# Kernel tuning notes

Measured on AMD Instinct MI355X. Metric: run time of the kernel, lower is better.

## Reference

```python
import jax, jax.numpy as jnp
import numpy as np

B, N, M = 8, 1024, 64          # graphs, ops/graph, machines/graph
OPF, MF = 16, 8                # raw feature dims
H, D, L = 8, 64, 3             # heads, head dim, HGT layers
F = H * D                      # 512 = hidden_dim * num_heads
KC = 8                         # compatible machines per op
NOP, NM = B * N, B * M
EPS = 1e-5


def _graph_ln(x, w, b):
    # PyG LayerNorm(mode='graph') with batch=None: scalar mean/std over the whole tensor
    x = x - x.mean()
    return x / (x.std() + EPS) * w + b


def _seg_softmax(a, idx, n):
    amax = jax.ops.segment_max(a, idx, num_segments=n)
    amax = jnp.where(jnp.isfinite(amax), amax, 0.0)
    ex = jnp.exp(a - amax[idx])
    s = jax.ops.segment_sum(ex, idx, num_segments=n)
    return ex / (s[idx] + 1e-16)


def _forward(op_x, machine_x, W_emb_op, b_emb_op, W_emb_m, b_emb_m,
             opn_w, opn_b, mn_w, mn_b, Wk, bk, Wq, bq, Wv, bv,
             A_rel, M_rel, p_rel, W_out, b_out, skip, ln_w, ln_b,
             ei_precedes, ei_canproc, ei_compat):
    x_op = _graph_ln(op_x @ W_emb_op + b_emb_op, opn_w, opn_b)
    x_m = _graph_ln(machine_x @ W_emb_m + b_emb_m, mn_w, mn_b)
    s0, d0 = ei_precedes   # op -> op
    s1, d1 = ei_canproc    # machine -> op
    s2, d2 = ei_compat     # op -> machine
    scale = 1.0 / jnp.sqrt(jnp.float32(D))
    for l in range(L):
        k_op = (x_op @ Wk[l, 0] + bk[l, 0]).reshape(NOP, H, D)
        q_op = (x_op @ Wq[l, 0] + bq[l, 0]).reshape(NOP, H, D)
        v_op = (x_op @ Wv[l, 0] + bv[l, 0]).reshape(NOP, H, D)
        k_m = (x_m @ Wk[l, 1] + bk[l, 1]).reshape(NM, H, D)
        q_m = (x_m @ Wq[l, 1] + bq[l, 1]).reshape(NM, H, D)
        v_m = (x_m @ Wv[l, 1] + bv[l, 1]).reshape(NM, H, D)
        # relation-specific per-head transforms (a_rel/m_rel of HGTConv)
        k0 = jnp.einsum('nhd,hde->nhe', k_op, A_rel[l, 0]); v0 = jnp.einsum('nhd,hde->nhe', v_op, M_rel[l, 0])
        k1 = jnp.einsum('nhd,hde->nhe', k_m, A_rel[l, 1]);  v1 = jnp.einsum('nhd,hde->nhe', v_m, M_rel[l, 1])
        k2 = jnp.einsum('nhd,hde->nhe', k_op, A_rel[l, 2]); v2 = jnp.einsum('nhd,hde->nhe', v_op, M_rel[l, 2])
        # attention into op nodes: joint softmax over both incoming edge types
        a0 = (q_op[d0] * k0[s0]).sum(-1) * p_rel[l, 0] * scale   # [E0,H]
        a1 = (q_op[d1] * k1[s1]).sum(-1) * p_rel[l, 1] * scale   # [E1,H]
        a_op = jnp.concatenate([a0, a1]); dd = jnp.concatenate([d0, d1])
        w = _seg_softmax(a_op, dd, NOP)
        msg = jnp.concatenate([v0[s0], v1[s1]]) * w[:, :, None]
        agg_op = jax.ops.segment_sum(msg, dd, num_segments=NOP).reshape(NOP, F)
        # attention into machine nodes
        a2 = (q_m[d2] * k2[s2]).sum(-1) * p_rel[l, 2] * scale
        w2 = _seg_softmax(a2, d2, NM)
        agg_m = jax.ops.segment_sum(v2[s2] * w2[:, :, None], d2, num_segments=NM).reshape(NM, F)
        # output projection + learned skip gate (HGTConv internals)
        o_op = jax.nn.gelu(agg_op, approximate=False) @ W_out[l, 0] + b_out[l, 0]
        o_m = jax.nn.gelu(agg_m, approximate=False) @ W_out[l, 1] + b_out[l, 1]
        g_op = jax.nn.sigmoid(skip[l, 0]); g_m = jax.nn.sigmoid(skip[l, 1])
        o_op = g_op * o_op + (1.0 - g_op) * x_op
        o_m = g_m * o_m + (1.0 - g_m) * x_m
        # wrapper residual + dropout(eval=identity) + graph layer norm
        x_op = _graph_ln(o_op + x_op, ln_w[l], ln_b[l])
        x_m = _graph_ln(o_m + x_m, ln_w[l], ln_b[l])
    fea_j = x_op.reshape(B, N, F)
    fea_m = x_m.reshape(B, M, F)
    return fea_j, fea_m, fea_j.mean(1, keepdims=True), fea_m.mean(1, keepdims=True)


def setup_inputs() -> dict:
    key = jax.random.key(0)
    ks = jax.random.split(key, 12)
    rng = np.random.default_rng(0)
    ids = np.arange(NOP).reshape(B, N)
    src0 = ids[:, :-1].ravel(); dst0 = ids[:, 1:].ravel()
    mach = rng.integers(0, M, size=(B, N, KC)) + (np.arange(B) * M)[:, None, None]
    ops = np.broadcast_to(ids[:, :, None], (B, N, KC))
    ei_precedes = jnp.asarray(np.stack([src0, dst0]), dtype=jnp.int32)
    ei_canproc = jnp.asarray(np.stack([mach.ravel(), ops.ravel()]), dtype=jnp.int32)
    ei_compat = jnp.asarray(np.stack([ops.ravel(), mach.ravel()]), dtype=jnp.int32)
    n = lambda k, sh, s=0.05: jax.random.normal(k, sh, dtype=jnp.float32) * s
    return dict(
        op_x=n(ks[0], (NOP, OPF), 1.0),
        machine_x=n(ks[1], (NM, MF), 1.0),
        W_emb_op=n(ks[2], (OPF, F)), b_emb_op=jnp.zeros((F,), jnp.float32),
        W_emb_m=n(ks[3], (MF, F)), b_emb_m=jnp.zeros((F,), jnp.float32),
        opn_w=jnp.ones((F,), jnp.float32), opn_b=jnp.zeros((F,), jnp.float32),
        mn_w=jnp.ones((F,), jnp.float32), mn_b=jnp.zeros((F,), jnp.float32),
        Wk=n(ks[4], (L, 2, F, F)), bk=jnp.zeros((L, 2, F), jnp.float32),
        Wq=n(ks[5], (L, 2, F, F)), bq=jnp.zeros((L, 2, F), jnp.float32),
        Wv=n(ks[6], (L, 2, F, F)), bv=jnp.zeros((L, 2, F), jnp.float32),
        A_rel=n(ks[7], (L, 3, H, D, D)), M_rel=n(ks[8], (L, 3, H, D, D)),
        p_rel=jnp.ones((L, 3, H), jnp.float32),
        W_out=n(ks[9], (L, 2, F, F)), b_out=jnp.zeros((L, 2, F), jnp.float32),
        skip=jnp.ones((L, 2), jnp.float32),
        ln_w=jnp.ones((L, F), jnp.float32), ln_b=jnp.zeros((L, F), jnp.float32),
        ei_precedes=ei_precedes, ei_canproc=ei_canproc, ei_compat=ei_compat,
    )


def reference(op_x, machine_x, W_emb_op, b_emb_op, W_emb_m, b_emb_m,
              opn_w, opn_b, mn_w, mn_b, Wk, bk, Wq, bq, Wv, bv,
              A_rel, M_rel, p_rel, W_out, b_out, skip, ln_w, ln_b,
              ei_precedes, ei_canproc, ei_compat):
    return _forward(op_x, machine_x, W_emb_op, b_emb_op, W_emb_m, b_emb_m,
                    opn_w, opn_b, mn_w, mn_b, Wk, bk, Wq, bq, Wv, bv,
                    A_rel, M_rel, p_rel, W_out, b_out, skip, ln_w, ln_b,
                    ei_precedes, ei_canproc, ei_compat)
```

## Files before the change

### kernel.cpp

```cpp
#include <hip/hip_runtime.h>

typedef unsigned short u16;
typedef __attribute__((ext_vector_type(4))) float floatx4;
typedef __attribute__((ext_vector_type(8))) short shortx8;
typedef __attribute__((ext_vector_type(4))) short shortx4;

#define NOPS 8192
#define NMS  512
#define CQ   2560
#define CM   1536
#define NE2  65536
#define TOPC (NOPS*512)
#define TMC  (NMS*512)

__device__ __forceinline__ float bf2f(u16 u){ return __uint_as_float(((unsigned)u)<<16); }
__device__ __forceinline__ u16 f2bf(float f){
  unsigned u = __float_as_uint(f);
  u += 0x7FFFu + ((u>>16)&1u);
  return (u16)(u>>16);
}
__device__ __forceinline__ float wred(float v){
  #pragma unroll
  for (int o=32;o;o>>=1) v += __shfl_xor(v,o,64);
  return v;
}
__device__ __forceinline__ float wredmax(float v){
  #pragma unroll
  for (int o=32;o;o>>=1) v = fmaxf(v, __shfl_xor(v,o,64));
  return v;
}
__device__ __forceinline__ float geluf(float x){
  return 0.5f*x*(1.f+erff(x*0.70710678118654752f));
}
__device__ __forceinline__ void block_stat_out2(float s, float s2, float* pstat, int slot){
  __shared__ float sb[8];
  s = wred(s); s2 = wred(s2);
  int wv = threadIdx.x >> 6;
  if ((threadIdx.x & 63) == 0){ sb[wv*2] = s; sb[wv*2+1] = s2; }
  __syncthreads();
  if (threadIdx.x == 0){
    float a = 0.f, b = 0.f;
    int nw = blockDim.x >> 6;
    for (int i=0;i<nw;++i){ a += sb[i*2]; b += sb[i*2+1]; }
    pstat[slot*2]   = a;
    pstat[slot*2+1] = b;
  }
}

__global__ __launch_bounds__(256) void cnt2_k(const int* __restrict__ s1, float* __restrict__ Ct,
                                              float* __restrict__ Cn){
  int idx = blockIdx.x*256 + threadIdx.x;
  int n = idx >> 6, l = idx & 63;
  const int* row = s1 + n*8;
  int cnt = 0;
  #pragma unroll
  for (int j=0;j<8;++j) cnt += ((row[j] & 63) == l);
  float f = (float)cnt;
  Cn[(size_t)n*64 + l] = f;
  int b = n >> 10, nl = n & 1023;
  Ct[(size_t)((b<<6) + l)*1024 + nl] = f;
}

__global__ __launch_bounds__(256) void tw_k(const float* __restrict__ Wout, const float* __restrict__ Wq,
                                            u16* __restrict__ Wout_t, u16* __restrict__ Wc_op_t,
                                            u16* __restrict__ Wc_m_t){
  __shared__ u16 t[64][65];
  int g = blockIdx.x;
  const float* s; u16* d;
  if (g < 6){
    s = Wout + (size_t)g*262144;
    d = Wout_t + (size_t)g*262144;
  } else {
    int blk = g - 6; int l = blk >> 1, side = blk & 1;
    s = Wq + (size_t)blk*262144;
    d = side ? (Wc_m_t + (size_t)l*CM*512) : (Wc_op_t + (size_t)l*CQ*512);
  }
  int kb = blockIdx.y*64, nb = blockIdx.z*64;
  int tx = threadIdx.x & 63, ty4 = threadIdx.x >> 6;
  #pragma unroll 4
  for (int p=0;p<16;++p){
    int k = ty4 + p*4;
    t[k][tx] = f2bf(s[(size_t)(kb+k)*512 + nb + tx]);
  }
  __syncthreads();
  #pragma unroll 4
  for (int p=0;p<16;++p){
    int n = ty4 + p*4;
    d[(size_t)(nb+n)*512 + kb + tx] = t[tx][n];
  }
}

__global__ void qb_k(const float* __restrict__ bq, float* bias_op, float* bias_m){
  int i = blockIdx.x*blockDim.x + threadIdx.x;
  if (i >= 3072) return;
  int l = i >> 10, side = (i >> 9) & 1, f = i & 511;
  float v = bq[(l*2+side)*512 + f];
  if (side==0) bias_op[l*CQ + f] = v; else bias_m[l*CM + f] = v;
}

__global__ __launch_bounds__(256) void combine3_k(const float* __restrict__ Wk, const float* __restrict__ Wv,
                                                  const float* __restrict__ Ar, const float* __restrict__ Mr,
                                                  u16* __restrict__ Wc_op_t, u16* __restrict__ Wc_m_t){
  __shared__ u16 As[64*72];
  __shared__ u16 Bs[128*72];
  int gx = blockIdx.x;
  int l = gx/48; int rem = gx - l*48; int s = rem >> 3; int h = rem & 7;
  int side = (s < 4) ? 0 : 1;
  int r = (s < 4) ? (s+1) : (s-3);
  int useK = side==0 ? (s==0 || s==2) : (s==4);
  int rel  = side==0 ? ((s<2)?0:2) : 1;
  const float* W   = (useK ? Wk : Wv) + (size_t)(l*2+side)*262144;
  const float* Rel = (useK ? Ar : Mr) + ((size_t)(l*3+rel)*8 + h)*4096;
  int h64 = h*64;
  u16* Wt = side ? (Wc_m_t + (size_t)l*CM*512) : (Wc_op_t + (size_t)l*CQ*512);
  int rbase = r*512 + h64;
  int cc0 = blockIdx.y * 128;
  int tid = threadIdx.x, lane = tid & 63, wave = tid >> 6;
  {
    int d = tid >> 2, e0 = (tid & 3) * 16;
    #pragma unroll
    for (int j=0;j<16;++j) As[(e0+j)*72 + d] = f2bf(Rel[d*64 + e0 + j]);
  }
  {
    int ccl = tid >> 1, d0 = (tid & 1) * 32;
    const float* src = W + (size_t)(cc0+ccl)*512 + h64 + d0;
    #pragma unroll
    for (int j=0;j<32;j+=4){
      floatx4 v = *(const floatx4*)(src + j);
      shortx4 sv;
      #pragma unroll
      for (int e=0;e<4;++e) sv[e] = (short)f2bf(v[e]);
      *(shortx4*)(Bs + ccl*72 + d0 + j) = sv;
    }
  }
  __syncthreads();
  int wm = wave & 1, wn = wave >> 1;
  int mrow = lane & 15, quad = lane >> 4;
  floatx4 acc[2][4];
  #pragma unroll
  for (int a=0;a<2;++a)
    #pragma unroll
    for (int b=0;b<4;++b) acc[a][b] = (floatx4){0.f,0.f,0.f,0.f};
  #pragma unroll
  for (int ks=0; ks<2; ++ks){
    shortx8 af[2], bf[4];
    #pragma unroll
    for (int mt=0;mt<2;++mt) af[mt] = *(const shortx8*)(As + (wm*32 + mt*16 + mrow)*72 + ks*32 + quad*8);
    #pragma unroll
    for (int nt=0;nt<4;++nt) bf[nt] = *(const shortx8*)(Bs + (wn*64 + nt*16 + mrow)*72 + ks*32 + quad*8);
    #pragma unroll
    for (int mt=0;mt<2;++mt)
      #pragma unroll
      for (int nt=0;nt<4;++nt)
        acc[mt][nt] = __builtin_amdgcn_mfma_f32_16x16x32_bf16(af[mt], bf[nt], acc[mt][nt], 0, 0, 0);
  }
  #pragma unroll
  for (int mt=0;mt<2;++mt){
    #pragma unroll
    for (int nt=0;nt<4;++nt){
      int ccl = wn*64 + nt*16 + mrow;
      #pragma unroll
      for (int r2=0;r2<4;++r2){
        int e = wm*32 + mt*16 + quad*4 + r2;
        Wt[(size_t)(rbase + e)*512 + cc0 + ccl] = f2bf(acc[mt][nt][r2]);
      }
    }
  }
}
__global__ void cbias_k(const float* __restrict__ bk, const float* __restrict__ bv,
                        const float* __restrict__ Ar, const float* __restrict__ Mr,
                        float* bias_op, float* bias_m){
  int gx = blockIdx.x; int e = threadIdx.x;
  int l = gx/48; int rem = gx - l*48; int s = rem >> 3; int h = rem & 7;
  int side = (s < 4) ? 0 : 1;
  int r = (s < 4) ? (s+1) : (s-3);
  int useK = side==0 ? (s==0 || s==2) : (s==4);
  int rel  = side==0 ? ((s<2)?0:2) : 1;
  const float* bb  = (useK ? bk : bv) + (size_t)(l*2+side)*512 + h*64;
  const float* Rel = (useK ? Ar : Mr) + ((size_t)(l*3+rel)*8 + h)*4096;
  float acc = 0.f;
  for (int d=0; d<64; ++d) acc += bb[d]*Rel[d*64 + e];
  float* bias = side ? (bias_m + l*CM) : (bias_op + l*CQ);
  bias[r*512 + h*64 + e] = acc;
}

__global__ __launch_bounds__(256) void embed2_k(const float* __restrict__ Xop, const float* __restrict__ Wop,
                                                const float* __restrict__ bop, float* __restrict__ Yop,
                                                const float* __restrict__ Xm, const float* __restrict__ Wm,
                                                const float* __restrict__ bm_, float* __restrict__ Ym,
                                                float* pstat, float* pstat_m){
  int bid = blockIdx.x;
  const float *X, *W, *bias; float *Y, *ps; int K, total, nb, lb;
  if (bid < 1024){ X=Xop; W=Wop; bias=bop; Y=Yop; ps=pstat;   K=16; total=TOPC; nb=1024; lb=bid; }
  else           { X=Xm;  W=Wm;  bias=bm_; Y=Ym;  ps=pstat_m; K=8;  total=TMC;  nb=128;  lb=bid-1024; }
  float s = 0.f, s2 = 0.f;
  for (int idx = lb*256 + threadIdx.x; idx < total; idx += nb*256){
    int n = idx >> 9, f = idx & 511;
    float v = bias[f];
    for (int c=0;c<K;++c) v += X[n*K+c] * W[c*512+f];
    Y[idx] = v;
    s += v; s2 += v*v;
  }
  block_stat_out2(s, s2, ps, lb);
}

__global__ __launch_bounds__(256) void ln2_k(const float* __restrict__ src_op, float* __restrict__ dst_op,
                                             u16* __restrict__ dbf_op, const float* __restrict__ w_op,
                                             const float* __restrict__ b_op,
                                             const float* __restrict__ src_m, float* __restrict__ dst_m,
                                             u16* __restrict__ dbf_m, const float* __restrict__ w_m,
                                             const float* __restrict__ b_m,
                                             const float* __restrict__ pstat, const float* __restrict__ pstat_m,
                                             int nbo, int nbm){
  int bid = blockIdx.x;
  const float *src, *w, *b, *ps; float* dst; u16* dbf; int total4, nb, lb, nblk; float inv_n;
  if (bid < 1024){ src=src_op; dst=dst_op; dbf=dbf_op; w=w_op; b=b_op; ps=pstat;
                   total4=TOPC/4; nb=1024; lb=bid; nblk=nbo; inv_n=1.f/TOPC; }
  else           { src=src_m;  dst=dst_m;  dbf=dbf_m;  w=w_m;  b=b_m;  ps=pstat_m;
                   total4=TMC/4;  nb=128;  lb=bid-1024; nblk=nbm; inv_n=1.f/TMC; }
  __shared__ float sb[8];
  __shared__ float mr[2];
  float s = 0.f, s2 = 0.f;
  for (int i = threadIdx.x; i < nblk; i += 256){ s += ps[2*i]; s2 += ps[2*i+1]; }
  s = wred(s); s2 = wred(s2);
  int wv = threadIdx.x >> 6;
  if ((threadIdx.x & 63) == 0){ sb[wv*2] = s; sb[wv*2+1] = s2; }
  __syncthreads();
  if (threadIdx.x == 0){
    float a = 0.f, bsum = 0.f;
    for (int i=0;i<4;++i){ a += sb[i*2]; bsum += sb[i*2+1]; }
    float mean = a * inv_n;
    float var  = fmaxf(bsum * inv_n - mean*mean, 0.f);
    mr[0] = mean;
    mr[1] = 1.f/(sqrtf(var) + 1e-5f);
  }
  __syncthreads();
  float mean = mr[0], rinv = mr[1];
  const floatx4* s4 = (const floatx4*)src;
  floatx4* d4 = (floatx4*)dst;
  shortx4* db4 = (shortx4*)dbf;
  const floatx4* w4 = (const floatx4*)w;
  const floatx4* b4 = (const floatx4*)b;
  for (int i = lb*256 + threadIdx.x; i < total4; i += nb*256){
    int f = i & 127;
    floatx4 v = s4[i], wv2 = w4[f], bv = b4[f];
    shortx4 sv;
    #pragma unroll
    for (int e=0;e<4;++e){ v[e] = (v[e]-mean)*rinv*wv2[e] + bv[e]; sv[e] = (short)f2bf(v[e]); }
    d4[i] = v;
    db4[i] = sv;
  }
}

__device__ __forceinline__ void gemm_gate_core(u16* As, u16* Bs, const u16* __restrict__ A,
                                               const u16* __restrict__ Bt,
                                               const float* __restrict__ xr, const float* __restrict__ bo,
                                               const float* __restrict__ sk, float* __restrict__ Y,
                                               float* pstat, int slot, int bx, int by){
  const int tid = threadIdx.x;
  const int lane = tid & 63, wave = tid >> 6;
  const int bm = by * 128, bn = bx * 128;
  const int wm = wave & 1, wn = wave >> 1;
  const int mrow = lane & 15, quad = lane >> 4;
  const u16* Ab = A + (size_t)bm*512;
  const u16* Bb = Bt + (size_t)bn*512;
  floatx4 acc[4][4];
  #pragma unroll
  for (int a=0;a<4;++a)
    #pragma unroll
    for (int b=0;b<4;++b) acc[a][b] = (floatx4){0.f,0.f,0.f,0.f};
  const int r0 = tid >> 2, c0 = (tid & 3) * 8;
  const int r1 = (tid+256) >> 2, c1 = ((tid+256) & 3) * 8;
  const int lds0 = wave*512;
  const int lds1 = wave*512 + 2048;
  for (int k0 = 0; k0 < 512; k0 += 32){
    __builtin_amdgcn_global_load_lds((const __attribute__((address_space(1))) void*)(Ab + (size_t)r0*512 + k0 + c0),
                                     (__attribute__((address_space(3))) void*)(As + lds0), 16, 0, 0);
    __builtin_amdgcn_global_load_lds((const __attribute__((address_space(1))) void*)(Ab + (size_t)r1*512 + k0 + c1),
                                     (__attribute__((address_space(3))) void*)(As + lds1), 16, 0, 0);
    __builtin_amdgcn_global_load_lds((const __attribute__((address_space(1))) void*)(Bb + (size_t)r0*512 + k0 + c0),
                                     (__attribute__((address_space(3))) void*)(Bs + lds0), 16, 0, 0);
    __builtin_amdgcn_global_load_lds((const __attribute__((address_space(1))) void*)(Bb + (size_t)r1*512 + k0 + c1),
                                     (__attribute__((address_space(3))) void*)(Bs + lds1), 16, 0, 0);
    __syncthreads();
    shortx8 af[4], bf[4];
    #pragma unroll
    for (int mt=0;mt<4;++mt) af[mt] = *(const shortx8*)(As + (wm*64 + mt*16 + mrow)*32 + quad*8);
    #pragma unroll
    for (int nt=0;nt<4;++nt) bf[nt] = *(const shortx8*)(Bs + (wn*64 + nt*16 + mrow)*32 + quad*8);
    #pragma unroll
    for (int mt=0;mt<4;++mt)
      #pragma unroll
      for (int nt=0;nt<4;++nt)
        acc[mt][nt] = __builtin_amdgcn_mfma_f32_16x16x32_bf16(af[mt], bf[nt], acc[mt][nt], 0, 0, 0);
    __syncthreads();
  }
  float g = 1.f/(1.f+expf(-(*sk)));
  float s = 0.f, s2 = 0.f;
  #pragma unroll
  for (int mt=0;mt<4;++mt){
    #pragma unroll
    for (int nt=0;nt<4;++nt){
      int col = bn + wn*64 + nt*16 + mrow;
      float bval = bo[col];
      #pragma unroll
      for (int r2=0;r2<4;++r2){
        int row = bm + wm*64 + mt*16 + quad*4 + r2;
        float v = acc[mt][nt][r2] + bval;
        float o = g*v + (2.f-g)*xr[(size_t)row*512 + col];
        Y[(size_t)row*512 + col] = o;
        s += o; s2 += o*o;
      }
    }
  }
  block_stat_out2(s, s2, pstat, slot);
}
__global__ __launch_bounds__(256) void gemmgate2_k(const u16* A1, const u16* B1, const float* x1,
                                                   const float* bo1, const float* sk1, float* Y1, float* ps1,
                                                   int nblk1,
                                                   const u16* A2, const u16* B2, const float* x2,
                                                   const float* bo2, const float* sk2, float* Y2, float* ps2){
  __shared__ u16 As[128*32];
  __shared__ u16 Bs[128*32];
  int id = blockIdx.x;
  if (id < nblk1) gemm_gate_core(As, Bs, A1, B1, x1, bo1, sk1, Y1, ps1, id, id % 4, id / 4);
  else { int j = id - nblk1; gemm_gate_core(As, Bs, A2, B2, x2, bo2, sk2, Y2, ps2, j, j % 4, j / 4); }
}

__device__ __forceinline__ void stage_half8(const u16* __restrict__ src, int kc, u16* region, int tid){
  int wave = tid >> 6;
  #pragma unroll
  for (int j=0;j<2;++j){
    int idx = j*512 + tid;
    int row = idx >> 2, qp2 = idx & 3;
    int qs = qp2 ^ (((row >> 3) & 1) << 1);
    __builtin_amdgcn_global_load_lds(
      (const __attribute__((address_space(1))) void*)(src + (size_t)row*512 + kc + qs*8),
      (__attribute__((address_space(3))) void*)(region + (j*512 + wave*64)*8),
      16, 0, 0);
  }
}

#define MFMA_QUAD(MH) do { \
  __builtin_amdgcn_s_barrier(); \
  asm volatile("s_waitcnt lgkmcnt(0)" ::: "memory"); \
  __builtin_amdgcn_sched_barrier(0); \
  __builtin_amdgcn_s_setprio(1); \
  _Pragma("unroll") \
  for (int mt=0;mt<4;++mt){ \
    _Pragma("unroll") \
    for (int nt=0;nt<4;++nt) \
      acc[(MH)*4+mt][nt] = __builtin_amdgcn_mfma_f32_16x16x32_bf16(af[mt], bf[nt], acc[(MH)*4+mt][nt], 0, 0, 0); \
  } \
  __builtin_amdgcn_s_setprio(0); \
} while(0)

__global__ __launch_bounds__(512, 2) void gemm8_k(
    const u16* __restrict__ A1, const u16* __restrict__ B1, const float* __restrict__ bias1,
    u16* __restrict__ C1, int N1, int nbx1, int nblk1,
    const u16* __restrict__ A2, const u16* __restrict__ B2, const float* __restrict__ bias2,
    u16* __restrict__ C2, int N2, int nbx2){
  extern __shared__ u16 lds[];
  int id = blockIdx.x;
  const u16 *A, *Bt; const float* bias; u16* C; int N, bx, by;
  if (id < nblk1){
    int xcd = id & 7, loc = id >> 3;
    int wg = xcd * (nblk1 >> 3) + loc;
    A=A1; Bt=B1; bias=bias1; C=C1; N=N1; bx=wg%nbx1; by=wg/nbx1;
  }
  else { int j=id-nblk1; A=A2; Bt=B2; bias=bias2; C=C2; N=N2; bx=j%nbx2; by=j/nbx2; }
  const int tid = threadIdx.x, lane = tid & 63, wave = tid >> 6;
  const int wm = wave & 1, wn = wave >> 1;
  const int mrow = lane & 15, quad = lane >> 4;
  const int qp = quad ^ ((mrow & 8) ? 2 : 0);
  const u16* Ab = A + (size_t)(by*256)*512;
  const u16* Bb = Bt + (size_t)(bx*256)*512;

  floatx4 acc[8][4];
  #pragma unroll
  for (int a=0;a<8;++a)
    #pragma unroll
    for (int b=0;b<4;++b) acc[a][b] = (floatx4){0.f,0.f,0.f,0.f};

  stage_half8(Ab, 0,  lds,          tid);
  stage_half8(Bb, 0,  lds + 16384,  tid);
  stage_half8(Ab, 32, lds + 8192,   tid);
  stage_half8(Bb, 32, lds + 24576,  tid);
  stage_half8(Ab, 64, lds + 32768,  tid);
  stage_half8(Bb, 64, lds + 49152,  tid);
  asm volatile("s_waitcnt vmcnt(8)" ::: "memory");
  __builtin_amdgcn_s_barrier();

  for (int t = 0; t < 8; ++t){
    const int s = t & 1;
    u16* Sbase = lds + s*32768;
    u16* Obase = lds + (s^1)*32768;
    const u16* a0 = Sbase + (wm*128 + mrow)*32 + qp*8;
    const u16* b0 = Sbase + 16384 + (wn*64 + mrow)*32 + qp*8;
    const int kc1 = ((t < 7) ? (t+1) : 7)*64 + 32;
    const int kc2 = ((t < 6) ? (t+2) : 7)*64;
    shortx8 af[4], bf[4];

    #pragma unroll
    for (int mt=0;mt<4;++mt) af[mt] = *(const shortx8*)(a0 + mt*512);
    #pragma unroll
    for (int nt=0;nt<4;++nt) bf[nt] = *(const shortx8*)(b0 + nt*512);
    stage_half8(Ab, kc1, Obase + 8192, tid);
    MFMA_QUAD(0);
    __builtin_amdgcn_s_barrier();

    #pragma unroll
    for (int mt=0;mt<4;++mt) af[mt] = *(const shortx8*)(a0 + 2048 + mt*512);
    stage_half8(Bb, kc1, Obase + 24576, tid);
    MFMA_QUAD(1);
    asm volatile("s_waitcnt vmcnt(8)" ::: "memory");
    __builtin_amdgcn_s_barrier();

    #pragma unroll
    for (int mt=0;mt<4;++mt) af[mt] = *(const shortx8*)(a0 + 8192 + mt*512);
    #pragma unroll
    for (int nt=0;nt<4;++nt) bf[nt] = *(const shortx8*)(b0 + 8192 + nt*512);
    stage_half8(Ab, kc2, Sbase, tid);
    MFMA_QUAD(0);
    __builtin_amdgcn_s_barrier();

    #pragma unroll
    for (int mt=0;mt<4;++mt) af[mt] = *(const shortx8*)(a0 + 8192 + 2048 + mt*512);
    stage_half8(Bb, kc2, Sbase + 16384, tid);
    MFMA_QUAD(1);
    asm volatile("s_waitcnt vmcnt(8)" ::: "memory");
    __builtin_amdgcn_s_barrier();
  }

  const int crow0 = by*256 + wm*128 + quad*4;
  const int ccol0 = bx*256 + wn*64 + mrow;
  float bv[4];
  #pragma unroll
  for (int nt=0;nt<4;++nt) bv[nt] = bias ? bias[ccol0 + nt*16] : 0.f;
  #pragma unroll
  for (int mh=0;mh<2;++mh){
    #pragma unroll
    for (int mt=0;mt<4;++mt){
      int row = crow0 + mh*64 + mt*16;
      #pragma unroll
      for (int nt=0;nt<4;++nt){
        int col = ccol0 + nt*16;
        #pragma unroll
        for (int r2=0;r2<4;++r2)
          C[(size_t)(row+r2)*N + col] = f2bf(acc[mh*4+mt][nt][r2] + bv[nt]);
      }
    }
  }
}

__global__ __launch_bounds__(256) void qk12_k(const u16* __restrict__ qkv_op, const u16* __restrict__ qkv_m,
                                              const float* __restrict__ prel, const float* __restrict__ Cn,
                                              float* __restrict__ S2f, u16* __restrict__ agg_op){
  __shared__ __align__(16) char smem[65536];
  u16* As = (u16*)smem;
  u16* Bs = As + 128*72;
  float* Sbuf = (float*)smem;
  u16* P     = (u16*)(smem + 36864);
  u16* v1T   = (u16*)(smem + 55296);
  float* linvS = (float*)(smem + 64512);
  float* wpreS = (float*)(smem + 65024);
  int bh = blockIdx.y; int b = bh >> 3, h = bh & 7;
  int n0 = blockIdx.x * 128;
  int tid = threadIdx.x, lane = tid & 63, wave = tid >> 6;
  int mrow = lane & 15, quad = lane >> 4;
  if (blockIdx.z == 0){
    int wm = wave & 1, wn = wave >> 1;
    float p1 = prel[8 + h] * 0.125f;
    {
      int row = tid >> 1, col = (tid & 1) * 32;
      const u16* src = qkv_op + (size_t)(b*1024 + n0 + row)*CQ + h*64 + col;
      #pragma unroll
      for (int e=0;e<4;++e) *(shortx8*)(As + row*72 + col + e*8) = *(const shortx8*)(src + e*8);
    }
    {
      int row = tid >> 2, col = (tid & 3) * 16;
      const u16* src = qkv_m + (size_t)(b*64 + row)*CM + 512 + h*64 + col;
      *(shortx8*)(Bs + row*72 + col)     = *(const shortx8*)(src);
      *(shortx8*)(Bs + row*72 + col + 8) = *(const shortx8*)(src + 8);
    }
    {
      int m = tid >> 2, dcol = (tid & 3) * 16;
      const u16* src = qkv_m + (size_t)(b*64 + m)*CM + 1024 + h*64 + dcol;
      shortx8 v0 = *(const shortx8*)(src);
      shortx8 v1 = *(const shortx8*)(src + 8);
      #pragma unroll
      for (int e=0;e<8;++e){ v1T[(dcol+e)*72 + m] = (u16)v0[e]; v1T[(dcol+8+e)*72 + m] = (u16)v1[e]; }
    }
    __syncthreads();
    floatx4 acc[4][2];
    #pragma unroll
    for (int a=0;a<4;++a){ acc[a][0] = (floatx4){0,0,0,0}; acc[a][1] = (floatx4){0,0,0,0}; }
    #pragma unroll
    for (int ks=0; ks<2; ++ks){
      shortx8 af[4], bf[2];
      #pragma unroll
      for (int mt=0;mt<4;++mt) af[mt] = *(const shortx8*)(As + (wm*64 + mt*16 + mrow)*72 + ks*32 + quad*8);
      #pragma unroll
      for (int nt=0;nt<2;++nt) bf[nt] = *(const shortx8*)(Bs + (wn*32 + nt*16 + mrow)*72 + ks*32 + quad*8);
      #pragma unroll
      for (int mt=0;mt<4;++mt)
        #pragma unroll
        for (int nt=0;nt<2;++nt)
          acc[mt][nt] = __builtin_amdgcn_mfma_f32_16x16x32_bf16(af[mt], bf[nt], acc[mt][nt], 0, 0, 0);
    }
    __syncthreads();
    #pragma unroll
    for (int mt=0;mt<4;++mt){
      #pragma unroll
      for (int nt=0;nt<2;++nt){
        int m = wn*32 + nt*16 + mrow;
        #pragma unroll
        for (int r2=0;r2<4;++r2){
          int nl = wm*64 + mt*16 + quad*4 + r2;
          Sbuf[nl*65 + m] = acc[mt][nt][r2] * p1;
        }
      }
    }
    __syncthreads();
    if (tid < 128){
      int n_g = b*1024 + n0 + tid;
      int nl  = n0 + tid;
      float sp = -1e30f;
      if (nl > 0){
        float p0 = prel[h] * 0.125f;
        const u16* qp = qkv_op + (size_t)n_g*CQ + h*64;
        const u16* kp = qkv_op + (size_t)(n_g-1)*CQ + 512 + h*64;
        float d = 0.f;
        #pragma unroll
        for (int j=0;j<8;++j){
          shortx8 qa = *(const shortx8*)(qp + j*8);
          shortx8 ka = *(const shortx8*)(kp + j*8);
          #pragma unroll
          for (int e=0;e<8;++e) d += bf2f((u16)qa[e])*bf2f((u16)ka[e]);
        }
        sp = d * p0;
      }
      const float* crow = Cn + (size_t)n_g*64;
      float mx = sp;
      #pragma unroll
      for (int m=0;m<64;++m){
        if (crow[m] > 0.f) mx = fmaxf(mx, Sbuf[tid*65 + m]);
      }
      float L = 0.f;
      u16* prow = P + tid*72;
      #pragma unroll
      for (int m0=0;m0<64;m0+=4){
        shortx4 pv;
        #pragma unroll
        for (int e=0;e<4;++e){
          float c = crow[m0+e];
          float w = (c > 0.f) ? c*expf(Sbuf[tid*65 + m0+e]-mx) : 0.f;
          L += w;
          pv[e] = (short)f2bf(w);
        }
        *(shortx4*)(prow + m0) = pv;
      }
      float ep = (nl > 0) ? expf(sp - mx) : 0.f;
      L += ep;
      wpreS[tid] = ep;
      linvS[tid] = 1.f/(L + 1e-16f);
    }
    __syncthreads();
    floatx4 po[4][2];
    #pragma unroll
    for (int a=0;a<4;++a){ po[a][0] = (floatx4){0,0,0,0}; po[a][1] = (floatx4){0,0,0,0}; }
    #pragma unroll
    for (int ks=0; ks<2; ++ks){
      shortx8 paf[4], pbf[2];
      #pragma unroll
      for (int mt=0;mt<4;++mt) paf[mt] = *(const shortx8*)(P + (wm*64 + mt*16 + mrow)*72 + ks*32 + quad*8);
      #pragma unroll
      for (int nt=0;nt<2;++nt) pbf[nt] = *(const shortx8*)(v1T + (wn*32 + nt*16 + mrow)*72 + ks*32 + quad*8);
      #pragma unroll
      for (int mt=0;mt<4;++mt)
        #pragma unroll
        for (int nt=0;nt<2;++nt)
          po[mt][nt] = __builtin_amdgcn_mfma_f32_16x16x32_bf16(paf[mt], pbf[nt], po[mt][nt], 0, 0, 0);
    }
    #pragma unroll
    for (int mt=0;mt<4;++mt){
      #pragma unroll
      for (int nt=0;nt<2;++nt){
        int d = wn*32 + nt*16 + mrow;
        #pragma unroll
        for (int r2=0;r2<4;++r2){
          int rl = wm*64 + mt*16 + quad*4 + r2;
          int n = n0 + rl;
          size_t ng = (size_t)b*1024 + n;
          float v = po[mt][nt][r2];
          if (n > 0) v += wpreS[rl] * bf2f(qkv_op[(ng-1)*CQ + 1024 + h*64 + d]);
          v *= linvS[rl];
          agg_op[ng*512 + h*64 + d] = f2bf(geluf(v));
        }
      }
    }
  } else {
    float p2 = prel[16 + h] * 0.125f;
    {
      int row = tid >> 2, col = (tid & 3) * 16;
      const u16* src = qkv_m + (size_t)(b*64+row)*CM + h*64 + col;
      *(shortx8*)(As + row*72 + col)     = *(const shortx8*)(src);
      *(shortx8*)(As + row*72 + col + 8) = *(const shortx8*)(src + 8);
    }
    {
      int row = tid >> 1, col = (tid & 1) * 32;
      const u16* src = qkv_op + (size_t)(b*1024 + n0 + row)*CQ + 1536 + h*64 + col;
      #pragma unroll
      for (int e=0;e<4;++e) *(shortx8*)(Bs + row*72 + col + e*8) = *(const shortx8*)(src + e*8);
    }
    __syncthreads();
    floatx4 acc[4][2];
    #pragma unroll
    for (int a=0;a<4;++a){ acc[a][0] = (floatx4){0,0,0,0}; acc[a][1] = (floatx4){0,0,0,0}; }
    #pragma unroll
    for (int ks=0; ks<2; ++ks){
      shortx8 af[4], bf[2];
      #pragma unroll
      for (int mt=0;mt<4;++mt) af[mt] = *(const shortx8*)(As + (mt*16 + mrow)*72 + ks*32 + quad*8);
      #pragma unroll
      for (int nt=0;nt<2;++nt) bf[nt] = *(const shortx8*)(Bs + (wave*32 + nt*16 + mrow)*72 + ks*32 + quad*8);
      #pragma unroll
      for (int mt=0;mt<4;++mt)
        #pragma unroll
        for (int nt=0;nt<2;++nt)
          acc[mt][nt] = __builtin_amdgcn_mfma_f32_16x16x32_bf16(af[mt], bf[nt], acc[mt][nt], 0, 0, 0);
    }
    #pragma unroll
    for (int mt=0;mt<4;++mt){
      #pragma unroll
      for (int nt=0;nt<2;++nt){
        int n = n0 + wave*32 + nt*16 + mrow;
        #pragma unroll
        for (int r2=0;r2<4;++r2){
          int m = mt*16 + quad*4 + r2;
          S2f[((size_t)(b*64 + m)*8 + h)*1024 + n] = acc[mt][nt][r2] * p2;
        }
      }
    }
  }
}

__global__ __launch_bounds__(512) void msoftm_k(const float* __restrict__ S2f, const float* __restrict__ Ct,
                                                u16* __restrict__ W2){
  int m = blockIdx.x;
  int h = threadIdx.x >> 6, d = threadIdx.x & 63;
  const float* srow = S2f + ((size_t)m*8 + h)*1024;
  const float* crow = Ct + (size_t)m*1024;
  float s[16], c[16];
  #pragma unroll
  for (int it=0; it<16; ++it){ s[it] = srow[it*64 + d]; c[it] = crow[it*64 + d]; }
  float mx = -1e30f;
  #pragma unroll
  for (int it=0; it<16; ++it) if (c[it] > 0.f) mx = fmaxf(mx, s[it]);
  mx = wredmax(mx);
  float e[16], L = 0.f;
  #pragma unroll
  for (int it=0; it<16; ++it){
    e[it] = (c[it] > 0.f) ? c[it]*expf(s[it]-mx) : 0.f;
    L += e[it];
  }
  L = wred(L);
  float inv = 1.f/(L + 1e-16f);
  u16* wrow = W2 + ((size_t)m*8 + h)*1024;
  #pragma unroll
  for (int it=0; it<16; ++it) wrow[it*64 + d] = f2bf(e[it]*inv);
}

__global__ __launch_bounds__(256) void aggm_k(const u16* __restrict__ qkv_op, const u16* __restrict__ W2,
                                              u16* __restrict__ agg_m){
  __shared__ u16 As[64*40];
  __shared__ u16 Bs[64*40];
  int bh = blockIdx.x; int b = bh >> 3, h = bh & 7;
  int tid = threadIdx.x, lane = tid & 63, wave = tid >> 6;
  int wm = wave & 1, wn = wave >> 1;
  int mrow = lane & 15, quad = lane >> 4;
  floatx4 acc[2][2];
  acc[0][0]=(floatx4){0,0,0,0}; acc[0][1]=(floatx4){0,0,0,0};
  acc[1][0]=(floatx4){0,0,0,0}; acc[1][1]=(floatx4){0,0,0,0};
  const int arow = tid >> 2, acol = (tid & 3) * 8;
  const int nrow = tid >> 3, dcol = (tid & 7) * 8;
  for (int ks = 0; ks < 32; ++ks){
    int nn0 = ks*32;
    *(shortx8*)(As + arow*40 + acol) =
        *(const shortx8*)(W2 + ((size_t)(b*64 + arow)*8 + h)*1024 + nn0 + acol);
    shortx8 vv = *(const shortx8*)(qkv_op + (size_t)(b*1024 + nn0 + nrow)*CQ + 2048 + h*64 + dcol);
    #pragma unroll
    for (int e=0;e<8;++e) Bs[(dcol+e)*40 + nrow] = (u16)vv[e];
    __syncthreads();
    shortx8 af[2], bf[2];
    #pragma unroll
    for (int mt=0;mt<2;++mt) af[mt] = *(const shortx8*)(As + (wm*32 + mt*16 + mrow)*40 + quad*8);
    #pragma unroll
    for (int nt=0;nt<2;++nt) bf[nt] = *(const shortx8*)(Bs + (wn*32 + nt*16 + mrow)*40 + quad*8);
    #pragma unroll
    for (int mt=0;mt<2;++mt)
      #pragma unroll
      for (int nt=0;nt<2;++nt)
        acc[mt][nt] = __builtin_amdgcn_mfma_f32_16x16x32_bf16(af[mt], bf[nt], acc[mt][nt], 0, 0, 0);
    __syncthreads();
  }
  #pragma unroll
  for (int mt=0;mt<2;++mt){
    #pragma unroll
    for (int nt=0;nt<2;++nt){
      int dd = wn*32 + nt*16 + mrow;
      #pragma unroll
      for (int r2=0;r2<4;++r2){
        int m = wm*32 + mt*16 + quad*4 + r2;
        agg_m[(size_t)(b*64 + m)*512 + h*64 + dd] = f2bf(geluf(acc[mt][nt][r2]));
      }
    }
  }
}

__global__ __launch_bounds__(512) void meanj_part_k(const float* __restrict__ xo, float* scratchJ){
  int b = blockIdx.x, chunk = blockIdx.y, f = threadIdx.x;
  float s = 0.f;
  for (int r=0;r<128;++r){
    int row = b*1024 + chunk*128 + r;
    s += xo[(size_t)row*512 + f];
  }
  scratchJ[(b*8 + chunk)*512 + f] = s;
}
__global__ __launch_bounds__(512) void mean2_k(const float* __restrict__ scratchJ, float* __restrict__ out){
  int i = blockIdx.x*512 + threadIdx.x;
  if (i < 4096){
    int b = i >> 9, f = i & 511;
    float s = 0.f;
    #pragma unroll
    for (int c=0;c<8;++c) s += scratchJ[(b*8+c)*512 + f];
    out[4456448 + i] = s * (1.f/1024.f);
  } else {
    int j = i - 4096;
    int b = j >> 9, f = j & 511;
    float s = 0.f;
    for (int r=0;r<64;++r) s += out[(size_t)TOPC + (size_t)(b*64+r)*512 + f];
    out[4460544 + j] = s * (1.f/64.f);
  }
}

extern "C" void kernel_launch(void* const* d_in, const int* in_sizes, int n_in,
                              void* d_out, int out_size, void* d_ws, size_t ws_size,
                              hipStream_t stream){
  const float* op_x      = (const float*)d_in[0];
  const float* machine_x = (const float*)d_in[1];
  const float* W_emb_op  = (const float*)d_in[2];
  const float* b_emb_op  = (const float*)d_in[3];
  const float* W_emb_m   = (const float*)d_in[4];
  const float* b_emb_m   = (const float*)d_in[5];
  const float* opn_w     = (const float*)d_in[6];
  const float* opn_b     = (const float*)d_in[7];
  const float* mn_w      = (const float*)d_in[8];
  const float* mn_b      = (const float*)d_in[9];
  const float* Wk        = (const float*)d_in[10];
  const float* bk        = (const float*)d_in[11];
  const float* Wq        = (const float*)d_in[12];
  const float* bq        = (const float*)d_in[13];
  const float* Wv        = (const float*)d_in[14];
  const float* bv        = (const float*)d_in[15];
  const float* A_rel     = (const float*)d_in[16];
  const float* M_rel     = (const float*)d_in[17];
  const float* p_rel     = (const float*)d_in[18];
  const float* W_out     = (const float*)d_in[19];
  const float* b_out     = (const float*)d_in[20];
  const float* skip      = (const float*)d_in[21];
  const float* ln_w      = (const float*)d_in[22];
  const float* ln_b      = (const float*)d_in[23];
  const int* s1          = (const int*)d_in[25];
  float* out = (float*)d_out;

  char* ws = (char*)d_ws;
  size_t off = 0;
  auto alloc = [&](size_t bytes)->void*{
    void* p = ws + off;
    off = (off + bytes + 255) & ~(size_t)255;
    return p;
  };
  float* pstat     = (float*)alloc(4096*4);
  float* scratchJ  = (float*)alloc(32768*4);
  float* Ct        = (float*)alloc((size_t)NMS*1024*4);
  float* Cn        = (float*)alloc((size_t)NOPS*64*4);
  float* S2f       = (float*)alloc((size_t)NMS*8*1024*4);
  u16*   W2        = (u16*)  alloc((size_t)NMS*8*1024*2);
  float* x_op      = (float*)alloc((size_t)NOPS*512*4);
  u16*   x_op_bf   = (u16*)  alloc((size_t)NOPS*512*2);
  float* x_m       = (float*)alloc((size_t)NMS*512*4);
  u16*   x_m_bf    = (u16*)  alloc((size_t)NMS*512*2);
  u16*   qkv_op    = (u16*)  alloc((size_t)NOPS*CQ*2);
  u16*   qkv_m     = (u16*)  alloc((size_t)NMS*CM*2);
  u16*   agg_op    = (u16*)  alloc((size_t)NOPS*512*2);
  u16*   agg_m     = (u16*)  alloc((size_t)NMS*512*2);
  u16*   Wc_op_t   = (u16*)  alloc((size_t)3*CQ*512*2);
  float* bias_op   = (float*)alloc((size_t)3*CQ*4);
  u16*   Wc_m_t    = (u16*)  alloc((size_t)3*CM*512*2);
  float* bias_m    = (float*)alloc((size_t)3*CM*4);
  u16*   Wout_t    = (u16*)  alloc((size_t)6*262144*2);
  float* o_op      = (float*)qkv_op;
  float* o_m       = (float*)qkv_m;
  float* pstat_m   = pstat + 2048;

  cnt2_k<<<2048,256,0,stream>>>(s1, Ct, Cn);
  tw_k<<<dim3(12,8,8),256,0,stream>>>(W_out, Wq, Wout_t, Wc_op_t, Wc_m_t);
  qb_k<<<12,256,0,stream>>>(bq, bias_op, bias_m);
  combine3_k<<<dim3(144,4),256,0,stream>>>(Wk, Wv, A_rel, M_rel, Wc_op_t, Wc_m_t);
  cbias_k<<<144,64,0,stream>>>(bk, bv, A_rel, M_rel, bias_op, bias_m);

  embed2_k<<<1152,256,0,stream>>>(op_x, W_emb_op, b_emb_op, x_op,
                                  machine_x, W_emb_m, b_emb_m, x_m, pstat, pstat_m);
  ln2_k<<<1152,256,0,stream>>>(x_op, x_op, x_op_bf, opn_w, opn_b,
                               x_m, x_m, x_m_bf, mn_w, mn_b, pstat, pstat_m, 1024, 128);

  for (int l=0; l<3; ++l){
    int last = (l == 2);
    gemm8_k<<<332,512,131072,stream>>>(x_op_bf, Wc_op_t + (size_t)l*CQ*512, bias_op + l*CQ, qkv_op, CQ, 10, 320,
                                       x_m_bf, Wc_m_t + (size_t)l*CM*512, bias_m + l*CM, qkv_m, CM, 6);
    qk12_k<<<dim3(8,64,2),256,0,stream>>>(qkv_op, qkv_m, p_rel + l*24, Cn, S2f, agg_op);
    msoftm_k<<<NMS,512,0,stream>>>(S2f, Ct, W2);
    aggm_k<<<64,256,0,stream>>>(qkv_op, W2, agg_m);
    gemmgate2_k<<<272,256,0,stream>>>(agg_op, Wout_t + (size_t)(l*2+0)*262144, x_op,
                                      b_out + (size_t)(l*2+0)*512, skip + l*2+0, o_op, pstat, 256,
                                      agg_m, Wout_t + (size_t)(l*2+1)*262144, x_m,
                                      b_out + (size_t)(l*2+1)*512, skip + l*2+1, o_m, pstat_m);
    ln2_k<<<1152,256,0,stream>>>(o_op, last ? out : x_op, x_op_bf, ln_w + l*512, ln_b + l*512,
                                 o_m, last ? (out + TOPC) : x_m, x_m_bf, ln_w + l*512, ln_b + l*512,
                                 pstat, pstat_m, 256, 16);
  }

  meanj_part_k<<<dim3(8,8),512,0,stream>>>(out, scratchJ);
  mean2_k<<<16,512,0,stream>>>(scratchJ, out);
}
```

Before: 630.7 us.

## Halve qk12 op tile to 64 rows and spread softmax across all threads

```diff
diff --git a/kernel.cpp b/kernel.cpp
--- a/kernel.cpp
+++ b/kernel.cpp
@@ -456,140 +456,143 @@
 __global__ __launch_bounds__(256) void qk12_k(const u16* __restrict__ qkv_op, const u16* __restrict__ qkv_m,
                                               const float* __restrict__ prel, const float* __restrict__ Cn,
                                               float* __restrict__ S2f, u16* __restrict__ agg_op){
-  __shared__ __align__(16) char smem[65536];
-  u16* As = (u16*)smem;
-  u16* Bs = As + 128*72;
+  __shared__ __align__(16) char smem[37376];
+  u16* smem16 = (u16*)smem;
+  u16* As = smem16;
+  u16* Bs = smem16 + 4608;
   float* Sbuf = (float*)smem;
-  u16* P     = (u16*)(smem + 36864);
-  u16* v1T   = (u16*)(smem + 55296);
-  float* linvS = (float*)(smem + 64512);
-  float* wpreS = (float*)(smem + 65024);
+  u16* P   = smem16 + 9216;
+  u16* v1T = smem16 + 13824;
+  float* wpreS = (float*)(smem + 36864);
+  float* linvS = (float*)(smem + 37120);
   int bh = blockIdx.y; int b = bh >> 3, h = bh & 7;
-  int n0 = blockIdx.x * 128;
+  int n0 = blockIdx.x * 64;
   int tid = threadIdx.x, lane = tid & 63, wave = tid >> 6;
   int mrow = lane & 15, quad = lane >> 4;
+  int wm = wave & 1, wn = wave >> 1;
+  int srow = tid >> 2, scol = (tid & 3) * 16;
   if (blockIdx.z == 0){
-    int wm = wave & 1, wn = wave >> 1;
     float p1 = prel[8 + h] * 0.125f;
     {
-      int row = tid >> 1, col = (tid & 1) * 32;
-      const u16* src = qkv_op + (size_t)(b*1024 + n0 + row)*CQ + h*64 + col;
-      #pragma unroll
-      for (int e=0;e<4;++e) *(shortx8*)(As + row*72 + col + e*8) = *(const shortx8*)(src + e*8);
+      const u16* src = qkv_op + (size_t)(b*1024 + n0 + srow)*CQ + h*64 + scol;
+      *(shortx8*)(As + srow*72 + scol)     = *(const shortx8*)(src);
+      *(shortx8*)(As + srow*72 + scol + 8) = *(const shortx8*)(src + 8);
     }
     {
-      int row = tid >> 2, col = (tid & 3) * 16;
-      const u16* src = qkv_m + (size_t)(b*64 + row)*CM + 512 + h*64 + col;
-      *(shortx8*)(Bs + row*72 + col)     = *(const shortx8*)(src);
-      *(shortx8*)(Bs + row*72 + col + 8) = *(const shortx8*)(src + 8);
+      const u16* src = qkv_m + (size_t)(b*64 + srow)*CM + 512 + h*64 + scol;
+      *(shortx8*)(Bs + srow*72 + scol)     = *(const shortx8*)(src);
+      *(shortx8*)(Bs + srow*72 + scol + 8) = *(const shortx8*)(src + 8);
     }
     {
-      int m = tid >> 2, dcol = (tid & 3) * 16;
-      const u16* src = qkv_m + (size_t)(b*64 + m)*CM + 1024 + h*64 + dcol;
+      const u16* src = qkv_m + (size_t)(b*64 + srow)*CM + 1024 + h*64 + scol;
       shortx8 v0 = *(const shortx8*)(src);
       shortx8 v1 = *(const shortx8*)(src + 8);
       #pragma unroll
-      for (int e=0;e<8;++e){ v1T[(dcol+e)*72 + m] = (u16)v0[e]; v1T[(dcol+8+e)*72 + m] = (u16)v1[e]; }
+      for (int e=0;e<8;++e){ v1T[(scol+e)*72 + srow] = (u16)v0[e]; v1T[(scol+8+e)*72 + srow] = (u16)v1[e]; }
     }
     __syncthreads();
-    floatx4 acc[4][2];
-    #pragma unroll
-    for (int a=0;a<4;++a){ acc[a][0] = (floatx4){0,0,0,0}; acc[a][1] = (floatx4){0,0,0,0}; }
+    floatx4 acc[2][2];
+    #pragma unroll
+    for (int a=0;a<2;++a){ acc[a][0] = (floatx4){0,0,0,0}; acc[a][1] = (floatx4){0,0,0,0}; }
     #pragma unroll
     for (int ks=0; ks<2; ++ks){
-      shortx8 af[4], bf[2];
-      #pragma unroll
-      for (int mt=0;mt<4;++mt) af[mt] = *(const shortx8*)(As + (wm*64 + mt*16 + mrow)*72 + ks*32 + quad*8);
+      shortx8 af[2], bf[2];
+      #pragma unroll
+      for (int mt=0;mt<2;++mt) af[mt] = *(const shortx8*)(As + (wm*32 + mt*16 + mrow)*72 + ks*32 + quad*8);
       #pragma unroll
       for (int nt=0;nt<2;++nt) bf[nt] = *(const shortx8*)(Bs + (wn*32 + nt*16 + mrow)*72 + ks*32 + quad*8);
       #pragma unroll
-      for (int mt=0;mt<4;++mt)
+      for (int mt=0;mt<2;++mt)
         #pragma unroll
         for (int nt=0;nt<2;++nt)
           acc[mt][nt] = __builtin_amdgcn_mfma_f32_16x16x32_bf16(af[mt], bf[nt], acc[mt][nt], 0, 0, 0);
     }
     __syncthreads();
     #pragma unroll
-    for (int mt=0;mt<4;++mt){
+    for (int mt=0;mt<2;++mt){
       #pragma unroll
       for (int nt=0;nt<2;++nt){
         int m = wn*32 + nt*16 + mrow;
         #pragma unroll
         for (int r2=0;r2<4;++r2){
-          int nl = wm*64 + mt*16 + quad*4 + r2;
-          Sbuf[nl*65 + m] = acc[mt][nt][r2] * p1;
+          int nl = wm*32 + mt*16 + quad*4 + r2;
+          Sbuf[nl*66 + m] = acc[mt][nt][r2] * p1;
         }
       }
     }
     __syncthreads();
-    if (tid < 128){
-      int n_g = b*1024 + n0 + tid;
-      int nl  = n0 + tid;
+    {
+      int row = srow;
+      int mb  = scol;
+      int n_g = b*1024 + n0 + row;
+      int nl  = n0 + row;
       float sp = -1e30f;
       if (nl > 0){
         float p0 = prel[h] * 0.125f;
-        const u16* qp = qkv_op + (size_t)n_g*CQ + h*64;
-        const u16* kp = qkv_op + (size_t)(n_g-1)*CQ + 512 + h*64;
+        const u16* qp = qkv_op + (size_t)n_g*CQ + h*64 + mb;
+        const u16* kp = qkv_op + (size_t)(n_g-1)*CQ + 512 + h*64 + mb;
+        shortx8 qa = *(const shortx8*)(qp), qb2 = *(const shortx8*)(qp + 8);
+        shortx8 ka = *(const shortx8*)(kp), kb2 = *(const shortx8*)(kp + 8);
         float d = 0.f;
         #pragma unroll
-        for (int j=0;j<8;++j){
-          shortx8 qa = *(const shortx8*)(qp + j*8);
-          shortx8 ka = *(const shortx8*)(kp + j*8);
-          #pragma unroll
-          for (int e=0;e<8;++e) d += bf2f((u16)qa[e])*bf2f((u16)ka[e]);
-        }
+        for (int e=0;e<8;++e) d += bf2f((u16)qa[e])*bf2f((u16)ka[e]) + bf2f((u16)qb2[e])*bf2f((u16)kb2[e]);
+        d += __shfl_xor(d, 1, 64);
+        d += __shfl_xor(d, 2, 64);
         sp = d * p0;
       }
-      const float* crow = Cn + (size_t)n_g*64;
+      const float* crow = Cn + (size_t)n_g*64 + mb;
+      float cv[16];
       float mx = sp;
       #pragma unroll
-      for (int m=0;m<64;++m){
-        if (crow[m] > 0.f) mx = fmaxf(mx, Sbuf[tid*65 + m]);
-      }
+      for (int j=0;j<16;++j){
+        cv[j] = crow[j];
+        if (cv[j] > 0.f) mx = fmaxf(mx, Sbuf[row*66 + mb + j]);
+      }
+      mx = fmaxf(mx, __shfl_xor(mx, 1, 64));
+      mx = fmaxf(mx, __shfl_xor(mx, 2, 64));
       float L = 0.f;
-      u16* prow = P + tid*72;
-      #pragma unroll
-      for (int m0=0;m0<64;m0+=4){
+      #pragma unroll
+      for (int j=0;j<16;j+=4){
         shortx4 pv;
         #pragma unroll
         for (int e=0;e<4;++e){
-          float c = crow[m0+e];
-          float w = (c > 0.f) ? c*expf(Sbuf[tid*65 + m0+e]-mx) : 0.f;
+          float w = (cv[j+e] > 0.f) ? cv[j+e]*expf(Sbuf[row*66 + mb + j + e] - mx) : 0.f;
           L += w;
           pv[e] = (short)f2bf(w);
         }
-        *(shortx4*)(prow + m0) = pv;
-      }
+        *(shortx4*)(P + row*72 + mb + j) = pv;
+      }
+      L += __shfl_xor(L, 1, 64);
+      L += __shfl_xor(L, 2, 64);
       float ep = (nl > 0) ? expf(sp - mx) : 0.f;
       L += ep;
-      wpreS[tid] = ep;
-      linvS[tid] = 1.f/(L + 1e-16f);
+      if ((tid & 3) == 0){ wpreS[row] = ep; linvS[row] = 1.f/(L + 1e-16f); }
     }
     __syncthreads();
-    floatx4 po[4][2];
-    #pragma unroll
-    for (int a=0;a<4;++a){ po[a][0] = (floatx4){0,0,0,0}; po[a][1] = (floatx4){0,0,0,0}; }
+    floatx4 po[2][2];
+    #pragma unroll
+    for (int a=0;a<2;++a){ po[a][0] = (floatx4){0,0,0,0}; po[a][1] = (floatx4){0,0,0,0}; }
     #pragma unroll
     for (int ks=0; ks<2; ++ks){
-      shortx8 paf[4], pbf[2];
-      #pragma unroll
-      for (int mt=0;mt<4;++mt) paf[mt] = *(const shortx8*)(P + (wm*64 + mt*16 + mrow)*72 + ks*32 + quad*8);
+      shortx8 paf[2], pbf[2];
+      #pragma unroll
+      for (int mt=0;mt<2;++mt) paf[mt] = *(const shortx8*)(P + (wm*32 + mt*16 + mrow)*72 + ks*32 + quad*8);
       #pragma unroll
       for (int nt=0;nt<2;++nt) pbf[nt] = *(const shortx8*)(v1T + (wn*32 + nt*16 + mrow)*72 + ks*32 + quad*8);
       #pragma unroll
-      for (int mt=0;mt<4;++mt)
+      for (int mt=0;mt<2;++mt)
         #pragma unroll
         for (int nt=0;nt<2;++nt)
           po[mt][nt] = __builtin_amdgcn_mfma_f32_16x16x32_bf16(paf[mt], pbf[nt], po[mt][nt], 0, 0, 0);
     }
     #pragma unroll
-    for (int mt=0;mt<4;++mt){
+    for (int mt=0;mt<2;++mt){
       #pragma unroll
       for (int nt=0;nt<2;++nt){
         int d = wn*32 + nt*16 + mrow;
         #pragma unroll
         for (int r2=0;r2<4;++r2){
-          int rl = wm*64 + mt*16 + quad*4 + r2;
+          int rl = wm*32 + mt*16 + quad*4 + r2;
           int n = n0 + rl;
           size_t ng = (size_t)b*1024 + n;
           float v = po[mt][nt][r2];
@@ -602,43 +605,41 @@
   } else {
     float p2 = prel[16 + h] * 0.125f;
     {
-      int row = tid >> 2, col = (tid & 3) * 16;
-      const u16* src = qkv_m + (size_t)(b*64+row)*CM + h*64 + col;
-      *(shortx8*)(As + row*72 + col)     = *(const shortx8*)(src);
-      *(shortx8*)(As + row*72 + col + 8) = *(const shortx8*)(src + 8);
+      const u16* src = qkv_m + (size_t)(b*64 + srow)*CM + h*64 + scol;
+      *(shortx8*)(As + srow*72 + scol)     = *(const shortx8*)(src);
+      *(shortx8*)(As + srow*72 + scol + 8) = *(const shortx8*)(src + 8);
     }
     {
-      int row = tid >> 1, col = (tid & 1) * 32;
-      const u16* src = qkv_op + (size_t)(b*1024 + n0 + row)*CQ + 1536 + h*64 + col;
-      #pragma unroll
-      for (int e=0;e<4;++e) *(shortx8*)(Bs + row*72 + col + e*8) = *(const shortx8*)(src + e*8);
+      const u16* src = qkv_op + (size_t)(b*1024 + n0 + srow)*CQ + 1536 + h*64 + scol;
+      *(shortx8*)(Bs + srow*72 + scol)     = *(const shortx8*)(src);
+      *(shortx8*)(Bs + srow*72 + scol + 8) = *(const shortx8*)(src + 8);
     }
     __syncthreads();
-    floatx4 acc[4][2];
-    #pragma unroll
-    for (int a=0;a<4;++a){ acc[a][0] = (floatx4){0,0,0,0}; acc[a][1] = (floatx4){0,0,0,0}; }
+    floatx4 acc[2][2];
+    #pragma unroll
+    for (int a=0;a<2;++a){ acc[a][0] = (floatx4){0,0,0,0}; acc[a][1] = (floatx4){0,0,0,0}; }
     #pragma unroll
     for (int ks=0; ks<2; ++ks){
-      shortx8 af[4], bf[2];
-      #pragma unroll
-      for (int mt=0;mt<4;++mt) af[mt] = *(const shortx8*)(As + (mt*16 + mrow)*72 + ks*32 + quad*8);
-      #pragma unroll
-      for (int nt=0;nt<2;++nt) bf[nt] = *(const shortx8*)(Bs + (wave*32 + nt*16 + mrow)*72 + ks*32 + quad*8);
-      #pragma unroll
-      for (int mt=0;mt<4;++mt)
+      shortx8 af[2], bf[2];
+      #pragma unroll
+      for (int mt=0;mt<2;++mt) af[mt] = *(const shortx8*)(As + (wm*32 + mt*16 + mrow)*72 + ks*32 + quad*8);
+      #pragma unroll
+      for (int nt=0;nt<2;++nt) bf[nt] = *(const shortx8*)(Bs + (wn*32 + nt*16 + mrow)*72 + ks*32 + quad*8);
+      #pragma unroll
+      for (int mt=0;mt<2;++mt)
         #pragma unroll
         for (int nt=0;nt<2;++nt)
           acc[mt][nt] = __builtin_amdgcn_mfma_f32_16x16x32_bf16(af[mt], bf[nt], acc[mt][nt], 0, 0, 0);
     }
     #pragma unroll
-    for (int mt=0;mt<4;++mt){
+    for (int mt=0;mt<2;++mt){
       #pragma unroll
       for (int nt=0;nt<2;++nt){
-        int n = n0 + wave*32 + nt*16 + mrow;
+        int n = wn*32 + nt*16 + mrow;
         #pragma unroll
         for (int r2=0;r2<4;++r2){
-          int m = mt*16 + quad*4 + r2;
-          S2f[((size_t)(b*64 + m)*8 + h)*1024 + n] = acc[mt][nt][r2] * p2;
+          int m = wm*32 + mt*16 + quad*4 + r2;
+          S2f[((size_t)(b*64 + m)*8 + h)*1024 + n0 + n] = acc[mt][nt][r2] * p2;
         }
       }
     }
@@ -819,7 +820,7 @@
     int last = (l == 2);
     gemm8_k<<<332,512,131072,stream>>>(x_op_bf, Wc_op_t + (size_t)l*CQ*512, bias_op + l*CQ, qkv_op, CQ, 10, 320,
                                        x_m_bf, Wc_m_t + (size_t)l*CM*512, bias_m + l*CM, qkv_m, CM, 6);
-    qk12_k<<<dim3(8,64,2),256,0,stream>>>(qkv_op, qkv_m, p_rel + l*24, Cn, S2f, agg_op);
+    qk12_k<<<dim3(16,64,2),256,0,stream>>>(qkv_op, qkv_m, p_rel + l*24, Cn, S2f, agg_op);
     msoftm_k<<<NMS,512,0,stream>>>(S2f, Ct, W2);
     aggm_k<<<64,256,0,stream>>>(qkv_op, W2, agg_m);
     gemmgate2_k<<<272,256,0,stream>>>(agg_op, Wout_t + (size_t)(l*2+0)*262144, x_op,
```

Result: faster. 589.1 us (-6.6%).
